# Kernel optimization log

Hardware: AMD Instinct MI355X
Metric: run time of the kernel (lower is better)

The kernel has to match this reference:

```python
import jax, jax.numpy as jnp
import numpy as np

N_NODES = 50000
N_EDGES = 800000
D_FEAT = 128
D_EMB = 128


def setup_inputs() -> dict:
    key = jax.random.key(0)
    k1, k2, k3, k4, k5 = jax.random.split(key, 5)
    feature = jax.random.normal(k1, (N_NODES, D_FEAT), dtype=jnp.float32)
    edge_src = jax.random.randint(k2, (N_EDGES,), 0, N_NODES, dtype=jnp.int32)
    edge_dst = jax.random.randint(k3, (N_EDGES,), 0, N_NODES, dtype=jnp.int32)
    edge_w = jax.random.uniform(k4, (N_EDGES,), dtype=jnp.float32)
    # reset_parameters: uniform(-stdv, stdv), stdv = 1/sqrt(embedding_size)
    stdv = 1.0 / np.sqrt(D_EMB)
    weight = jax.random.uniform(k5, (D_FEAT, D_EMB), dtype=jnp.float32,
                                minval=-stdv, maxval=stdv)
    return {"feature": feature, "edge_src": edge_src, "edge_dst": edge_dst,
            "edge_w": edge_w, "weight": weight}


def reference(feature, edge_src, edge_dst, edge_w, weight):
    # spmm(adj, feature): out[dst] += w * feature[src]
    msgs = edge_w[:, None] * feature[edge_src]          # [E, D_FEAT]
    agg = jax.ops.segment_sum(msgs, edge_dst, num_segments=feature.shape[0])
    # residual blend then dense projection
    blended = 0.5 * agg + 0.5 * feature                  # [N, D_FEAT]
    return blended @ weight                              # [N, D_EMB]
```

## Files before the change

kernel.cpp:

```cpp
#include <hip/hip_runtime.h>

#define N_NODES 50000
#define N_EDGES 800000
#define D 128
#define NBUCK 196
#define CAP 4800
#define CHUNK 4096
#define PA_BLKS ((N_EDGES + CHUNK - 1) / CHUNK)
#define FB_BLKS 12500
#define WT_BLKS 64

typedef __attribute__((ext_vector_type(8))) short short8;
typedef __attribute__((ext_vector_type(4))) float f32x4;

__device__ __forceinline__ unsigned short f2bf(float f) {
    unsigned u = __float_as_uint(f);
    u += 0x7fff + ((u >> 16) & 1);
    return (unsigned short)(u >> 16);
}
__device__ __forceinline__ float lo16f(unsigned u) { return __uint_as_float(u << 16); }
__device__ __forceinline__ float hi16f(unsigned u) { return __uint_as_float(u & 0xffff0000u); }

__global__ __launch_bounds__(256) void prep_passA(
    const float2* __restrict__ feat2, unsigned* __restrict__ fb,
    const float* __restrict__ W, unsigned short* __restrict__ Wt,
    const int* __restrict__ esrc, const int* __restrict__ edst,
    const float* __restrict__ ew, int* __restrict__ gcur,
    uint2* __restrict__ tmp) {
    __shared__ int lh[NBUCK], lbase[NBUCK], lcur[NBUCK];
    int blk = blockIdx.x, t = threadIdx.x;

    if (blk >= PA_BLKS) {
        int b2 = blk - PA_BLKS;
        if (b2 < FB_BLKS) {
            int i = b2 * 256 + t;
            float2 f = feat2[i];
            fb[i] = (unsigned)f2bf(f.x) | ((unsigned)f2bf(f.y) << 16);
        } else {
            int idx = (b2 - FB_BLKS) * 256 + t;
            int n = idx >> 7, k = idx & 127;
            Wt[idx] = f2bf(W[k * 128 + n]);
        }
        return;
    }

    for (int i = t; i < NBUCK; i += 256) lh[i] = 0;
    __syncthreads();
    int e0 = blk * CHUNK;
    unsigned key[16];
    float wv[16];
#pragma unroll
    for (int j = 0; j < 16; ++j) {
        int e = e0 + j * 256 + t;
        if (e < N_EDGES) {
            int src = esrc[e], dd = edst[e];
            key[j] = (unsigned)src | ((unsigned)(dd & 255) << 16) |
                     ((unsigned)(dd >> 8) << 24);
            wv[j] = ew[e];
            atomicAdd(&lh[dd >> 8], 1);
        } else key[j] = 0xff000000u;
    }
    __syncthreads();
    for (int i = t; i < NBUCK; i += 256) {
        lbase[i] = atomicAdd(&gcur[i], lh[i]);
        lcur[i] = 0;
    }
    __syncthreads();
#pragma unroll
    for (int j = 0; j < 16; ++j) {
        int b = key[j] >> 24;
        if (b < NBUCK) {
            int r = atomicAdd(&lcur[b], 1);
            tmp[(size_t)b * CAP + lbase[b] + r] =
                make_uint2(key[j] & 0x00ffffffu, __float_as_uint(wv[j]));
        }
    }
}

__global__ __launch_bounds__(256) void passB(const int* __restrict__ gcur,
                                             const uint2* __restrict__ tmp,
                                             int* __restrict__ offsets,
                                             uint2* __restrict__ sw) {
    __shared__ int hist[256], ps[256];
    __shared__ int sbase, scnt;
    int b = blockIdx.x, t = threadIdx.x;

    int gv = (t < NBUCK) ? gcur[t] : 0;
    ps[t] = gv;
    __syncthreads();
    for (int off = 1; off < 256; off <<= 1) {
        int x = (t >= off) ? ps[t - off] : 0;
        __syncthreads();
        ps[t] += x;
        __syncthreads();
    }
    if (t == b) { sbase = ps[t] - gv; scnt = gv; }
    hist[t] = 0;
    __syncthreads();
    int base = sbase, cnt = scnt;
    const uint2* seg = tmp + (size_t)b * CAP;

    for (int i = t; i < cnt; i += 256) atomicAdd(&hist[seg[i].x >> 16], 1);
    __syncthreads();
    int h = hist[t];
    ps[t] = h;
    __syncthreads();
    for (int off = 1; off < 256; off <<= 1) {
        int x = (t >= off) ? ps[t - off] : 0;
        __syncthreads();
        ps[t] += x;
        __syncthreads();
    }
    int o = base + ps[t] - h;
    int node = b * 256 + t;
    if (node < N_NODES) offsets[node] = o;
    if (b == NBUCK - 1 && t == 0) offsets[N_NODES] = N_EDGES;
    __syncthreads();
    hist[t] = o;
    __syncthreads();
    for (int i = t; i < cnt; i += 256) {
        uint2 u = seg[i];
        int pos = atomicAdd(&hist[u.x >> 16], 1);
        sw[pos] = make_uint2(u.x & 0xffffu, u.y);
    }
}

__global__ __launch_bounds__(256, 2) void agg_gemm(const int* __restrict__ offsets,
                                                   const uint2* __restrict__ sw,
                                                   const unsigned* __restrict__ fb,
                                                   const unsigned short* __restrict__ Wt,
                                                   float* __restrict__ out) {
    __shared__ unsigned Arows[16][68];
    int wave = threadIdx.x >> 6;
    int lane = threadIdx.x & 63;
    int row0 = blockIdx.x * 16;

#pragma unroll 1
    for (int i = 0; i < 4; ++i) {
        int n = __builtin_amdgcn_readfirstlane(row0 + wave * 4 + i);
        int b = offsets[n], e2 = offsets[n + 1];
        unsigned us = fb[(size_t)n * 64 + lane];
        float ax = 0.f, ay = 0.f;
        int e = b;
        int nfull = (e2 - b) >> 4;

        uint2 p[16];
        {
            int rem = e2 - e;
#pragma unroll
            for (int j = 0; j < 16; ++j) {
                int idx = (j < rem) ? j : (rem > 0 ? rem - 1 : 0);
                p[j] = sw[e + idx];
            }
        }
#pragma unroll 1
        for (int t = 0; t < nfull; ++t) {
            unsigned u[16];
#pragma unroll
            for (int j = 0; j < 16; ++j) u[j] = fb[(size_t)p[j].x * 64 + lane];
            int en = e + 16;
            int rem = e2 - en;
            uint2 pn[16];
#pragma unroll
            for (int j = 0; j < 16; ++j) {
                int idx = (j < rem) ? j : (rem > 0 ? rem - 1 : 0);
                pn[j] = sw[en + idx];
            }
#pragma unroll
            for (int j = 0; j < 16; ++j) {
                float w = __uint_as_float(p[j].y);
                ax += w * lo16f(u[j]);
                ay += w * hi16f(u[j]);
            }
#pragma unroll
            for (int j = 0; j < 16; ++j) p[j] = pn[j];
            e = en;
        }
        int rem = e2 - e;
        if (rem > 0) {
            unsigned u[16];
#pragma unroll
            for (int j = 0; j < 16; ++j) u[j] = fb[(size_t)p[j].x * 64 + lane];
#pragma unroll
            for (int j = 0; j < 16; ++j) {
                float w = (j < rem) ? __uint_as_float(p[j].y) : 0.f;
                ax += w * lo16f(u[j]);
                ay += w * hi16f(u[j]);
            }
        }
        float rx = 0.5f * (ax + lo16f(us));
        float ry = 0.5f * (ay + hi16f(us));
        Arows[wave * 4 + i][lane] = (unsigned)f2bf(rx) | ((unsigned)f2bf(ry) << 16);
    }
    __syncthreads();

    int quad = lane >> 4;
    int col  = lane & 15;
    short8 a[4];
#pragma unroll
    for (int kk = 0; kk < 4; ++kk)
        a[kk] = *reinterpret_cast<const short8*>(&Arows[col][kk * 16 + quad * 4]);

#pragma unroll
    for (int ii = 0; ii < 2; ++ii) {
        int n0 = wave * 2 + ii;
        const short8* bp = reinterpret_cast<const short8*>(Wt) + ((n0 * 16 + col) * 16 + quad);
        f32x4 acc = {0.f, 0.f, 0.f, 0.f};
        acc = __builtin_amdgcn_mfma_f32_16x16x32_bf16(a[0], bp[0],  acc, 0, 0, 0);
        acc = __builtin_amdgcn_mfma_f32_16x16x32_bf16(a[1], bp[4],  acc, 0, 0, 0);
        acc = __builtin_amdgcn_mfma_f32_16x16x32_bf16(a[2], bp[8],  acc, 0, 0, 0);
        acc = __builtin_amdgcn_mfma_f32_16x16x32_bf16(a[3], bp[12], acc, 0, 0, 0);
#pragma unroll
        for (int rr = 0; rr < 4; ++rr)
            out[(size_t)(row0 + quad * 4 + rr) * D + n0 * 16 + col] = acc[rr];
    }
}

extern "C" void kernel_launch(void* const* d_in, const int* in_sizes, int n_in,
                              void* d_out, int out_size, void* d_ws, size_t ws_size,
                              hipStream_t stream) {
    const float* feat = (const float*)d_in[0];
    const int*   esrc = (const int*)d_in[1];
    const int*   edst = (const int*)d_in[2];
    const float* ew   = (const float*)d_in[3];
    const float* W    = (const float*)d_in[4];
    float*       out  = (float*)d_out;

    char* ws = (char*)d_ws;
    uint2*          sw      = (uint2*)(ws + 0);
    unsigned*       fb      = (unsigned*)(ws + 6400000);
    int*            offsets = (int*)(ws + 19200000);
    unsigned short* Wt      = (unsigned short*)(ws + 19400064);
    int*            gcur    = (int*)(ws + 19432832);
    uint2* tmp = (uint2*)d_out;

    hipMemsetAsync(gcur, 0, NBUCK * sizeof(int), stream);
    prep_passA<<<PA_BLKS + FB_BLKS + WT_BLKS, 256, 0, stream>>>(
        (const float2*)feat, fb, W, Wt, esrc, edst, ew, gcur, tmp);
    passB<<<NBUCK, 256, 0, stream>>>(gcur, tmp, offsets, sw);
    agg_gemm<<<N_NODES / 16, 256, 0, stream>>>(offsets, sw, fb, Wt, out);
}
```

Measured before the change: 151.5 us.

## Replace two-level bucket sort with global histogram, scan, and atomic scatter CSR build

```diff
diff --git a/kernel.cpp b/kernel.cpp
--- a/kernel.cpp
+++ b/kernel.cpp
@@ -3,12 +3,12 @@
 #define N_NODES 50000
 #define N_EDGES 800000
 #define D 128
-#define NBUCK 196
-#define CAP 4800
-#define CHUNK 4096
-#define PA_BLKS ((N_EDGES + CHUNK - 1) / CHUNK)
+#define H_BLKS 782
+#define SC_BLKS 782
 #define FB_BLKS 12500
 #define WT_BLKS 64
+#define SCAN_BLKS 196
+#define HIST_PAD 50176
 
 typedef __attribute__((ext_vector_type(8))) short short8;
 typedef __attribute__((ext_vector_type(4))) float f32x4;
@@ -21,72 +21,51 @@
 __device__ __forceinline__ float lo16f(unsigned u) { return __uint_as_float(u << 16); }
 __device__ __forceinline__ float hi16f(unsigned u) { return __uint_as_float(u & 0xffff0000u); }
 
-__global__ __launch_bounds__(256) void prep_passA(
+__global__ __launch_bounds__(256) void prep_hist(
     const float2* __restrict__ feat2, unsigned* __restrict__ fb,
     const float* __restrict__ W, unsigned short* __restrict__ Wt,
-    const int* __restrict__ esrc, const int* __restrict__ edst,
-    const float* __restrict__ ew, int* __restrict__ gcur,
-    uint2* __restrict__ tmp) {
-    __shared__ int lh[NBUCK], lbase[NBUCK], lcur[NBUCK];
+    const int* __restrict__ edst, int* __restrict__ hist) {
     int blk = blockIdx.x, t = threadIdx.x;
-
-    if (blk >= PA_BLKS) {
-        int b2 = blk - PA_BLKS;
-        if (b2 < FB_BLKS) {
-            int i = b2 * 256 + t;
-            float2 f = feat2[i];
-            fb[i] = (unsigned)f2bf(f.x) | ((unsigned)f2bf(f.y) << 16);
-        } else {
-            int idx = (b2 - FB_BLKS) * 256 + t;
-            int n = idx >> 7, k = idx & 127;
-            Wt[idx] = f2bf(W[k * 128 + n]);
+    if (blk < H_BLKS) {
+        int e0 = blk * 1024 + t;
+#pragma unroll
+        for (int j = 0; j < 4; ++j) {
+            int e = e0 + j * 256;
+            if (e < N_EDGES) atomicAdd(&hist[edst[e]], 1);
         }
         return;
     }
-
-    for (int i = t; i < NBUCK; i += 256) lh[i] = 0;
-    __syncthreads();
-    int e0 = blk * CHUNK;
-    unsigned key[16];
-    float wv[16];
-#pragma unroll
-    for (int j = 0; j < 16; ++j) {
-        int e = e0 + j * 256 + t;
-        if (e < N_EDGES) {
-            int src = esrc[e], dd = edst[e];
-            key[j] = (unsigned)src | ((unsigned)(dd & 255) << 16) |
-                     ((unsigned)(dd >> 8) << 24);
-            wv[j] = ew[e];
-            atomicAdd(&lh[dd >> 8], 1);
-        } else key[j] = 0xff000000u;
-    }
-    __syncthreads();
-    for (int i = t; i < NBUCK; i += 256) {
-        lbase[i] = atomicAdd(&gcur[i], lh[i]);
-        lcur[i] = 0;
-    }
-    __syncthreads();
-#pragma unroll
-    for (int j = 0; j < 16; ++j) {
-        int b = key[j] >> 24;
-        if (b < NBUCK) {
-            int r = atomicAdd(&lcur[b], 1);
-            tmp[(size_t)b * CAP + lbase[b] + r] =
-                make_uint2(key[j] & 0x00ffffffu, __float_as_uint(wv[j]));
-        }
-    }
-}
-
-__global__ __launch_bounds__(256) void passB(const int* __restrict__ gcur,
-                                             const uint2* __restrict__ tmp,
-                                             int* __restrict__ offsets,
-                                             uint2* __restrict__ sw) {
-    __shared__ int hist[256], ps[256];
-    __shared__ int sbase, scnt;
+    int b2 = blk - H_BLKS;
+    if (b2 < FB_BLKS) {
+        int i = b2 * 256 + t;
+        float2 f = feat2[i];
+        fb[i] = (unsigned)f2bf(f.x) | ((unsigned)f2bf(f.y) << 16);
+    } else {
+        int idx = (b2 - FB_BLKS) * 256 + t;
+        int n = idx >> 7, k = idx & 127;
+        Wt[idx] = f2bf(W[k * 128 + n]);
+    }
+}
+
+__global__ __launch_bounds__(256) void scan_all(const int* __restrict__ hist,
+                                                int* __restrict__ offsets,
+                                                int* __restrict__ cur) {
+    __shared__ int ps[256];
     int b = blockIdx.x, t = threadIdx.x;
 
-    int gv = (t < NBUCK) ? gcur[t] : 0;
-    ps[t] = gv;
+    int acc = 0;
+    for (int i = t; i < b * 256; i += 256) acc += hist[i];
+    ps[t] = acc;
+    __syncthreads();
+    for (int off = 128; off > 0; off >>= 1) {
+        if (t < off) ps[t] += ps[t + off];
+        __syncthreads();
+    }
+    int base = ps[0];
+    __syncthreads();
+
+    int v = hist[b * 256 + t];
+    ps[t] = v;
     __syncthreads();
     for (int off = 1; off < 256; off <<= 1) {
         int x = (t >= off) ? ps[t - off] : 0;
@@ -94,34 +73,29 @@
         ps[t] += x;
         __syncthreads();
     }
-    if (t == b) { sbase = ps[t] - gv; scnt = gv; }
-    hist[t] = 0;
-    __syncthreads();
-    int base = sbase, cnt = scnt;
-    const uint2* seg = tmp + (size_t)b * CAP;
-
-    for (int i = t; i < cnt; i += 256) atomicAdd(&hist[seg[i].x >> 16], 1);
-    __syncthreads();
-    int h = hist[t];
-    ps[t] = h;
-    __syncthreads();
-    for (int off = 1; off < 256; off <<= 1) {
-        int x = (t >= off) ? ps[t - off] : 0;
-        __syncthreads();
-        ps[t] += x;
-        __syncthreads();
-    }
-    int o = base + ps[t] - h;
-    int node = b * 256 + t;
-    if (node < N_NODES) offsets[node] = o;
-    if (b == NBUCK - 1 && t == 0) offsets[N_NODES] = N_EDGES;
-    __syncthreads();
-    hist[t] = o;
-    __syncthreads();
-    for (int i = t; i < cnt; i += 256) {
-        uint2 u = seg[i];
-        int pos = atomicAdd(&hist[u.x >> 16], 1);
-        sw[pos] = make_uint2(u.x & 0xffffu, u.y);
+    int o = base + ps[t] - v;
+    int n = b * 256 + t;
+    if (n < N_NODES) {
+        offsets[n] = o;
+        cur[n] = o;
+    }
+    if (b == SCAN_BLKS - 1 && t == 0) offsets[N_NODES] = N_EDGES;
+}
+
+__global__ __launch_bounds__(256) void scatter(const int* __restrict__ esrc,
+                                               const int* __restrict__ edst,
+                                               const float* __restrict__ ew,
+                                               int* __restrict__ cur,
+                                               uint2* __restrict__ sw) {
+    int e0 = blockIdx.x * 1024 + threadIdx.x;
+#pragma unroll
+    for (int j = 0; j < 4; ++j) {
+        int e = e0 + j * 256;
+        if (e < N_EDGES) {
+            int d = edst[e];
+            int pos = atomicAdd(&cur[d], 1);
+            sw[pos] = make_uint2((unsigned)esrc[e], __float_as_uint(ew[e]));
+        }
     }
 }
 
@@ -231,12 +205,13 @@
     unsigned*       fb      = (unsigned*)(ws + 6400000);
     int*            offsets = (int*)(ws + 19200000);
     unsigned short* Wt      = (unsigned short*)(ws + 19400064);
-    int*            gcur    = (int*)(ws + 19432832);
-    uint2* tmp = (uint2*)d_out;
-
-    hipMemsetAsync(gcur, 0, NBUCK * sizeof(int), stream);
-    prep_passA<<<PA_BLKS + FB_BLKS + WT_BLKS, 256, 0, stream>>>(
-        (const float2*)feat, fb, W, Wt, esrc, edst, ew, gcur, tmp);
-    passB<<<NBUCK, 256, 0, stream>>>(gcur, tmp, offsets, sw);
+    int* hist = (int*)d_out;
+    int* cur  = (int*)((char*)d_out + 200704);
+
+    hipMemsetAsync(hist, 0, HIST_PAD * sizeof(int), stream);
+    prep_hist<<<H_BLKS + FB_BLKS + WT_BLKS, 256, 0, stream>>>(
+        (const float2*)feat, fb, W, Wt, edst, hist);
+    scan_all<<<SCAN_BLKS, 256, 0, stream>>>(hist, offsets, cur);
+    scatter<<<SC_BLKS, 256, 0, stream>>>(esrc, edst, ew, cur, sw);
     agg_gemm<<<N_NODES / 16, 256, 0, stream>>>(offsets, sw, fb, Wt, out);
 }
```

New measurement: 241.5 us. 59.5% more time.

## Fuse bucket sort, aggregation and GEMM into one cooperative kernel with LDS accumulators

Applied to the files above, without the earlier changes.

```diff
diff --git a/kernel.cpp b/kernel.cpp
--- a/kernel.cpp
+++ b/kernel.cpp
@@ -1,4 +1,5 @@
 #include <hip/hip_runtime.h>
+#include <hip/hip_cooperative_groups.h>
 
 #define N_NODES 50000
 #define N_EDGES 800000
@@ -9,6 +10,8 @@
 #define PA_BLKS ((N_EDGES + CHUNK - 1) / CHUNK)
 #define FB_BLKS 12500
 #define WT_BLKS 64
+#define APAD 132
+#define LDS_BYTES (256 * APAD * 4)
 
 typedef __attribute__((ext_vector_type(8))) short short8;
 typedef __attribute__((ext_vector_type(4))) float f32x4;
@@ -77,142 +80,125 @@
     }
 }
 
-__global__ __launch_bounds__(256) void passB(const int* __restrict__ gcur,
-                                             const uint2* __restrict__ tmp,
-                                             int* __restrict__ offsets,
-                                             uint2* __restrict__ sw) {
-    __shared__ int hist[256], ps[256];
-    __shared__ int sbase, scnt;
-    int b = blockIdx.x, t = threadIdx.x;
-
-    int gv = (t < NBUCK) ? gcur[t] : 0;
-    ps[t] = gv;
-    __syncthreads();
-    for (int off = 1; off < 256; off <<= 1) {
-        int x = (t >= off) ? ps[t - off] : 0;
-        __syncthreads();
-        ps[t] += x;
-        __syncthreads();
-    }
-    if (t == b) { sbase = ps[t] - gv; scnt = gv; }
-    hist[t] = 0;
-    __syncthreads();
-    int base = sbase, cnt = scnt;
+__global__ __launch_bounds__(1024) void agg_fused(
+    const int* __restrict__ gcur, const uint2* __restrict__ tmp,
+    const unsigned* __restrict__ fb, const unsigned short* __restrict__ Wt,
+    float* __restrict__ out) {
+    extern __shared__ float acc[];
+    int t = threadIdx.x;
+    int w = t >> 6;
+    int lane = t & 63;
+    int b = blockIdx.x;
+
+    for (int i = t; i < 256 * APAD; i += 1024) acc[i] = 0.f;
+    __syncthreads();
+
+    int cnt = gcur[b];
     const uint2* seg = tmp + (size_t)b * CAP;
-
-    for (int i = t; i < cnt; i += 256) atomicAdd(&hist[seg[i].x >> 16], 1);
-    __syncthreads();
-    int h = hist[t];
-    ps[t] = h;
-    __syncthreads();
-    for (int off = 1; off < 256; off <<= 1) {
-        int x = (t >= off) ? ps[t - off] : 0;
-        __syncthreads();
-        ps[t] += x;
-        __syncthreads();
-    }
-    int o = base + ps[t] - h;
-    int node = b * 256 + t;
-    if (node < N_NODES) offsets[node] = o;
-    if (b == NBUCK - 1 && t == 0) offsets[N_NODES] = N_EDGES;
-    __syncthreads();
-    hist[t] = o;
-    __syncthreads();
-    for (int i = t; i < cnt; i += 256) {
-        uint2 u = seg[i];
-        int pos = atomicAdd(&hist[u.x >> 16], 1);
-        sw[pos] = make_uint2(u.x & 0xffffu, u.y);
-    }
-}
-
-__global__ __launch_bounds__(256, 2) void agg_gemm(const int* __restrict__ offsets,
-                                                   const uint2* __restrict__ sw,
-                                                   const unsigned* __restrict__ fb,
-                                                   const unsigned short* __restrict__ Wt,
-                                                   float* __restrict__ out) {
-    __shared__ unsigned Arows[16][68];
-    int wave = threadIdx.x >> 6;
-    int lane = threadIdx.x & 63;
-    int row0 = blockIdx.x * 16;
-
+    unsigned dummy_kx = ((unsigned)(w * 16)) << 16;
+
+    for (int c = 0; c < cnt; c += 64) {
+        int idx = c + lane;
+        uint2 kv = seg[idx < cnt ? idx : cnt - 1];
+        int dl = (kv.x >> 16);
+        bool own = (idx < cnt) && ((dl >> 4) == w);
+        unsigned long long m = __ballot(own);
+        while (m) {
+            unsigned kx[4], ky[4];
+#pragma unroll
+            for (int q = 0; q < 4; ++q) {
+                if (m) {
+                    int sq = __builtin_ctzll(m);
+                    m &= m - 1;
+                    kx[q] = (unsigned)__builtin_amdgcn_readlane((int)kv.x, sq);
+                    ky[q] = (unsigned)__builtin_amdgcn_readlane((int)kv.y, sq);
+                } else {
+                    kx[q] = dummy_kx;
+                    ky[q] = 0u;
+                }
+            }
+            int r0 = kx[0] >> 16, r1 = kx[1] >> 16, r2 = kx[2] >> 16, r3 = kx[3] >> 16;
+            unsigned u0 = fb[(size_t)(kx[0] & 0xffffu) * 64 + lane];
+            unsigned u1 = fb[(size_t)(kx[1] & 0xffffu) * 64 + lane];
+            unsigned u2 = fb[(size_t)(kx[2] & 0xffffu) * 64 + lane];
+            unsigned u3 = fb[(size_t)(kx[3] & 0xffffu) * 64 + lane];
+            float w0 = __uint_as_float(ky[0]), w1 = __uint_as_float(ky[1]);
+            float w2 = __uint_as_float(ky[2]), w3 = __uint_as_float(ky[3]);
+            float cx0 = w0 * lo16f(u0), cy0 = w0 * hi16f(u0);
+            float cx1 = w1 * lo16f(u1), cy1 = w1 * hi16f(u1);
+            float cx2 = w2 * lo16f(u2), cy2 = w2 * hi16f(u2);
+            float cx3 = w3 * lo16f(u3), cy3 = w3 * hi16f(u3);
+            bool v1 = true, v2 = true, v3 = true;
+            if (r1 == r0) { cx0 += cx1; cy0 += cy1; v1 = false; }
+            if (r2 == r0) { cx0 += cx2; cy0 += cy2; v2 = false; }
+            else if (v1 && r2 == r1) { cx1 += cx2; cy1 += cy2; v2 = false; }
+            if (r3 == r0) { cx0 += cx3; cy0 += cy3; v3 = false; }
+            else if (v1 && r3 == r1) { cx1 += cx3; cy1 += cy3; v3 = false; }
+            else if (v2 && r3 == r2) { cx2 += cx3; cy2 += cy3; v3 = false; }
+            {
+                float2* p = (float2*)(acc + r0 * APAD) + lane;
+                float2 v = *p; v.x += cx0; v.y += cy0; *p = v;
+            }
+            if (v1) {
+                float2* p = (float2*)(acc + r1 * APAD) + lane;
+                float2 v = *p; v.x += cx1; v.y += cy1; *p = v;
+            }
+            if (v2) {
+                float2* p = (float2*)(acc + r2 * APAD) + lane;
+                float2 v = *p; v.x += cx2; v.y += cy2; *p = v;
+            }
+            if (v3) {
+                float2* p = (float2*)(acc + r3 * APAD) + lane;
+                float2 v = *p; v.x += cx3; v.y += cy3; *p = v;
+            }
+        }
+    }
+    __syncthreads();
+
+    for (int i = t; i < 256 * 64; i += 1024) {
+        int r = i >> 6, c = i & 63;
+        int node = b * 256 + r;
+        unsigned uf = (node < N_NODES) ? fb[(size_t)node * 64 + c] : 0u;
+        float2* p = (float2*)(acc + r * APAD) + c;
+        float2 v = *p;
+        v.x = 0.5f * (v.x + lo16f(uf));
+        v.y = 0.5f * (v.y + hi16f(uf));
+        *p = v;
+    }
+    __syncthreads();
+
+    cooperative_groups::this_grid().sync();
+
+    int quad = lane >> 4;
+    int col = lane & 15;
+    const float* arow = acc + (w * 16 + col) * APAD;
+    short8 a[4];
+#pragma unroll
+    for (int kk = 0; kk < 4; ++kk) {
+        int k0 = kk * 32 + quad * 8;
+        f32x4 x0 = *reinterpret_cast<const f32x4*>(arow + k0);
+        f32x4 x1 = *reinterpret_cast<const f32x4*>(arow + k0 + 4);
+        short8 af;
+        af[0] = (short)f2bf(x0[0]); af[1] = (short)f2bf(x0[1]);
+        af[2] = (short)f2bf(x0[2]); af[3] = (short)f2bf(x0[3]);
+        af[4] = (short)f2bf(x1[0]); af[5] = (short)f2bf(x1[1]);
+        af[6] = (short)f2bf(x1[2]); af[7] = (short)f2bf(x1[3]);
+        a[kk] = af;
+    }
 #pragma unroll 1
-    for (int i = 0; i < 4; ++i) {
-        int n = __builtin_amdgcn_readfirstlane(row0 + wave * 4 + i);
-        int b = offsets[n], e2 = offsets[n + 1];
-        unsigned us = fb[(size_t)n * 64 + lane];
-        float ax = 0.f, ay = 0.f;
-        int e = b;
-        int nfull = (e2 - b) >> 4;
-
-        uint2 p[16];
-        {
-            int rem = e2 - e;
-#pragma unroll
-            for (int j = 0; j < 16; ++j) {
-                int idx = (j < rem) ? j : (rem > 0 ? rem - 1 : 0);
-                p[j] = sw[e + idx];
-            }
-        }
-#pragma unroll 1
-        for (int t = 0; t < nfull; ++t) {
-            unsigned u[16];
-#pragma unroll
-            for (int j = 0; j < 16; ++j) u[j] = fb[(size_t)p[j].x * 64 + lane];
-            int en = e + 16;
-            int rem = e2 - en;
-            uint2 pn[16];
-#pragma unroll
-            for (int j = 0; j < 16; ++j) {
-                int idx = (j < rem) ? j : (rem > 0 ? rem - 1 : 0);
-                pn[j] = sw[en + idx];
-            }
-#pragma unroll
-            for (int j = 0; j < 16; ++j) {
-                float w = __uint_as_float(p[j].y);
-                ax += w * lo16f(u[j]);
-                ay += w * hi16f(u[j]);
-            }
-#pragma unroll
-            for (int j = 0; j < 16; ++j) p[j] = pn[j];
-            e = en;
-        }
-        int rem = e2 - e;
-        if (rem > 0) {
-            unsigned u[16];
-#pragma unroll
-            for (int j = 0; j < 16; ++j) u[j] = fb[(size_t)p[j].x * 64 + lane];
-#pragma unroll
-            for (int j = 0; j < 16; ++j) {
-                float w = (j < rem) ? __uint_as_float(p[j].y) : 0.f;
-                ax += w * lo16f(u[j]);
-                ay += w * hi16f(u[j]);
-            }
-        }
-        float rx = 0.5f * (ax + lo16f(us));
-        float ry = 0.5f * (ay + hi16f(us));
-        Arows[wave * 4 + i][lane] = (unsigned)f2bf(rx) | ((unsigned)f2bf(ry) << 16);
-    }
-    __syncthreads();
-
-    int quad = lane >> 4;
-    int col  = lane & 15;
-    short8 a[4];
-#pragma unroll
-    for (int kk = 0; kk < 4; ++kk)
-        a[kk] = *reinterpret_cast<const short8*>(&Arows[col][kk * 16 + quad * 4]);
-
-#pragma unroll
-    for (int ii = 0; ii < 2; ++ii) {
-        int n0 = wave * 2 + ii;
+    for (int n0 = 0; n0 < 8; ++n0) {
         const short8* bp = reinterpret_cast<const short8*>(Wt) + ((n0 * 16 + col) * 16 + quad);
-        f32x4 acc = {0.f, 0.f, 0.f, 0.f};
-        acc = __builtin_amdgcn_mfma_f32_16x16x32_bf16(a[0], bp[0],  acc, 0, 0, 0);
-        acc = __builtin_amdgcn_mfma_f32_16x16x32_bf16(a[1], bp[4],  acc, 0, 0, 0);
-        acc = __builtin_amdgcn_mfma_f32_16x16x32_bf16(a[2], bp[8],  acc, 0, 0, 0);
-        acc = __builtin_amdgcn_mfma_f32_16x16x32_bf16(a[3], bp[12], acc, 0, 0, 0);
-#pragma unroll
-        for (int rr = 0; rr < 4; ++rr)
-            out[(size_t)(row0 + quad * 4 + rr) * D + n0 * 16 + col] = acc[rr];
+        f32x4 accv = {0.f, 0.f, 0.f, 0.f};
+        accv = __builtin_amdgcn_mfma_f32_16x16x32_bf16(a[0], bp[0],  accv, 0, 0, 0);
+        accv = __builtin_amdgcn_mfma_f32_16x16x32_bf16(a[1], bp[4],  accv, 0, 0, 0);
+        accv = __builtin_amdgcn_mfma_f32_16x16x32_bf16(a[2], bp[8],  accv, 0, 0, 0);
+        accv = __builtin_amdgcn_mfma_f32_16x16x32_bf16(a[3], bp[12], accv, 0, 0, 0);
+#pragma unroll
+        for (int rr = 0; rr < 4; ++rr) {
+            int node = b * 256 + w * 16 + quad * 4 + rr;
+            if (node < N_NODES)
+                out[(size_t)node * D + n0 * 16 + col] = accv[rr];
+        }
     }
 }
 
@@ -227,16 +213,28 @@
     float*       out  = (float*)d_out;
 
     char* ws = (char*)d_ws;
-    uint2*          sw      = (uint2*)(ws + 0);
-    unsigned*       fb      = (unsigned*)(ws + 6400000);
-    int*            offsets = (int*)(ws + 19200000);
-    unsigned short* Wt      = (unsigned short*)(ws + 19400064);
-    int*            gcur    = (int*)(ws + 19432832);
+    unsigned*       fb   = (unsigned*)(ws + 6400000);
+    unsigned short* Wt   = (unsigned short*)(ws + 19400064);
+    int*            gcur = (int*)(ws + 19432832);
     uint2* tmp = (uint2*)d_out;
+
+    static int attr_set = 0;
+    if (!attr_set) {
+        hipFuncSetAttribute((const void*)agg_fused,
+                            hipFuncAttributeMaxDynamicSharedMemorySize, LDS_BYTES);
+        attr_set = 1;
+    }
 
     hipMemsetAsync(gcur, 0, NBUCK * sizeof(int), stream);
     prep_passA<<<PA_BLKS + FB_BLKS + WT_BLKS, 256, 0, stream>>>(
         (const float2*)feat, fb, W, Wt, esrc, edst, ew, gcur, tmp);
-    passB<<<NBUCK, 256, 0, stream>>>(gcur, tmp, offsets, sw);
-    agg_gemm<<<N_NODES / 16, 256, 0, stream>>>(offsets, sw, fb, Wt, out);
-}
+
+    const int* gcur_c = gcur;
+    const uint2* tmp_c = tmp;
+    const unsigned* fb_c = fb;
+    const unsigned short* Wt_c = Wt;
+    void* kargs[] = {(void*)&gcur_c, (void*)&tmp_c, (void*)&fb_c, (void*)&Wt_c,
+                     (void*)&out};
+    hipLaunchCooperativeKernel((void*)agg_fused, dim3(NBUCK), dim3(1024), kargs,
+                               LDS_BYTES, stream);
+}
```

New measurement: 263.2 us. 73.8% more time.

## Use 1024-thread blocks for prep and bucket-scatter passes

Applied to the files above, without the earlier changes.

```diff
diff --git a/kernel.cpp b/kernel.cpp
--- a/kernel.cpp
+++ b/kernel.cpp
@@ -7,8 +7,8 @@
 #define CAP 4800
 #define CHUNK 4096
 #define PA_BLKS ((N_EDGES + CHUNK - 1) / CHUNK)
-#define FB_BLKS 12500
-#define WT_BLKS 64
+#define FB_BLKS 3125
+#define WT_BLKS 16
 
 typedef __attribute__((ext_vector_type(8))) short short8;
 typedef __attribute__((ext_vector_type(4))) float f32x4;
@@ -21,7 +21,7 @@
 __device__ __forceinline__ float lo16f(unsigned u) { return __uint_as_float(u << 16); }
 __device__ __forceinline__ float hi16f(unsigned u) { return __uint_as_float(u & 0xffff0000u); }
 
-__global__ __launch_bounds__(256) void prep_passA(
+__global__ __launch_bounds__(1024) void prep_passA(
     const float2* __restrict__ feat2, unsigned* __restrict__ fb,
     const float* __restrict__ W, unsigned short* __restrict__ Wt,
     const int* __restrict__ esrc, const int* __restrict__ edst,
@@ -33,25 +33,25 @@
     if (blk >= PA_BLKS) {
         int b2 = blk - PA_BLKS;
         if (b2 < FB_BLKS) {
-            int i = b2 * 256 + t;
+            int i = b2 * 1024 + t;
             float2 f = feat2[i];
             fb[i] = (unsigned)f2bf(f.x) | ((unsigned)f2bf(f.y) << 16);
         } else {
-            int idx = (b2 - FB_BLKS) * 256 + t;
+            int idx = (b2 - FB_BLKS) * 1024 + t;
             int n = idx >> 7, k = idx & 127;
             Wt[idx] = f2bf(W[k * 128 + n]);
         }
         return;
     }
 
-    for (int i = t; i < NBUCK; i += 256) lh[i] = 0;
+    for (int i = t; i < NBUCK; i += 1024) lh[i] = 0;
     __syncthreads();
     int e0 = blk * CHUNK;
-    unsigned key[16];
-    float wv[16];
-#pragma unroll
-    for (int j = 0; j < 16; ++j) {
-        int e = e0 + j * 256 + t;
+    unsigned key[4];
+    float wv[4];
+#pragma unroll
+    for (int j = 0; j < 4; ++j) {
+        int e = e0 + j * 1024 + t;
         if (e < N_EDGES) {
             int src = esrc[e], dd = edst[e];
             key[j] = (unsigned)src | ((unsigned)(dd & 255) << 16) |
@@ -61,13 +61,13 @@
         } else key[j] = 0xff000000u;
     }
     __syncthreads();
-    for (int i = t; i < NBUCK; i += 256) {
+    for (int i = t; i < NBUCK; i += 1024) {
         lbase[i] = atomicAdd(&gcur[i], lh[i]);
         lcur[i] = 0;
     }
     __syncthreads();
 #pragma unroll
-    for (int j = 0; j < 16; ++j) {
+    for (int j = 0; j < 4; ++j) {
         int b = key[j] >> 24;
         if (b < NBUCK) {
             int r = atomicAdd(&lcur[b], 1);
@@ -77,48 +77,49 @@
     }
 }
 
-__global__ __launch_bounds__(256) void passB(const int* __restrict__ gcur,
-                                             const uint2* __restrict__ tmp,
-                                             int* __restrict__ offsets,
-                                             uint2* __restrict__ sw) {
+__global__ __launch_bounds__(1024) void passB(const int* __restrict__ gcur,
+                                              const uint2* __restrict__ tmp,
+                                              int* __restrict__ offsets,
+                                              uint2* __restrict__ sw) {
     __shared__ int hist[256], ps[256];
-    __shared__ int sbase, scnt;
     int b = blockIdx.x, t = threadIdx.x;
 
-    int gv = (t < NBUCK) ? gcur[t] : 0;
-    ps[t] = gv;
+    if (t < 256) ps[t] = (t < b) ? gcur[t] : 0;
+    __syncthreads();
+    for (int off = 128; off > 0; off >>= 1) {
+        if (t < off) ps[t] += ps[t + off];
+        __syncthreads();
+    }
+    int base = ps[0];
+    int cnt = gcur[b];
+    if (t < 256) hist[t] = 0;
+    __syncthreads();
+
+    const uint2* seg = tmp + (size_t)b * CAP;
+    for (int i = t; i < cnt; i += 1024) atomicAdd(&hist[seg[i].x >> 16], 1);
+    __syncthreads();
+
+    int h = 0;
+    if (t < 256) { h = hist[t]; ps[t] = h; }
     __syncthreads();
     for (int off = 1; off < 256; off <<= 1) {
-        int x = (t >= off) ? ps[t - off] : 0;
+        int x = 0;
+        if (t < 256 && t >= off) x = ps[t - off];
         __syncthreads();
-        ps[t] += x;
+        if (t < 256) ps[t] += x;
         __syncthreads();
     }
-    if (t == b) { sbase = ps[t] - gv; scnt = gv; }
-    hist[t] = 0;
-    __syncthreads();
-    int base = sbase, cnt = scnt;
-    const uint2* seg = tmp + (size_t)b * CAP;
-
-    for (int i = t; i < cnt; i += 256) atomicAdd(&hist[seg[i].x >> 16], 1);
-    __syncthreads();
-    int h = hist[t];
-    ps[t] = h;
-    __syncthreads();
-    for (int off = 1; off < 256; off <<= 1) {
-        int x = (t >= off) ? ps[t - off] : 0;
-        __syncthreads();
-        ps[t] += x;
-        __syncthreads();
-    }
-    int o = base + ps[t] - h;
-    int node = b * 256 + t;
-    if (node < N_NODES) offsets[node] = o;
+    int o = 0;
+    if (t < 256) {
+        o = base + ps[t] - h;
+        int node = b * 256 + t;
+        if (node < N_NODES) offsets[node] = o;
+    }
     if (b == NBUCK - 1 && t == 0) offsets[N_NODES] = N_EDGES;
     __syncthreads();
-    hist[t] = o;
-    __syncthreads();
-    for (int i = t; i < cnt; i += 256) {
+    if (t < 256) hist[t] = o;
+    __syncthreads();
+    for (int i = t; i < cnt; i += 1024) {
         uint2 u = seg[i];
         int pos = atomicAdd(&hist[u.x >> 16], 1);
         sw[pos] = make_uint2(u.x & 0xffffu, u.y);
@@ -235,8 +236,8 @@
     uint2* tmp = (uint2*)d_out;
 
     hipMemsetAsync(gcur, 0, NBUCK * sizeof(int), stream);
-    prep_passA<<<PA_BLKS + FB_BLKS + WT_BLKS, 256, 0, stream>>>(
+    prep_passA<<<PA_BLKS + FB_BLKS + WT_BLKS, 1024, 0, stream>>>(
         (const float2*)feat, fb, W, Wt, esrc, edst, ew, gcur, tmp);
-    passB<<<NBUCK, 256, 0, stream>>>(gcur, tmp, offsets, sw);
+    passB<<<NBUCK, 1024, 0, stream>>>(gcur, tmp, offsets, sw);
     agg_gemm<<<N_NODES / 16, 256, 0, stream>>>(offsets, sw, fb, Wt, out);
 }
```

Measured after the change: 146.5 us. -3.3%, faster.
